# Performance work log

Hardware: AMD Instinct MI355X
Metric: run time of the kernel (lower is better)

Reference implementation:

```python
import jax, jax.numpy as jnp
import numpy as np

L = 4096      # number of nodes (treated as sequence length, batch=1)
D = 256       # in_channels == out_channels
H = 8         # heads
DH = D // H   # head dim = 32
NUM_EDGE_TYPES = 14


def setup_inputs() -> dict:
    key = jax.random.key(0)
    ks = jax.random.split(key, 7)
    x = jax.random.normal(ks[0], (L, D), dtype=jnp.float32)
    mask = jax.random.randint(ks[1], (L, L), 0, NUM_EDGE_TYPES, dtype=jnp.int64)
    s = 1.0 / np.sqrt(D)
    in_proj_w = jax.random.uniform(ks[2], (3 * D, D), jnp.float32, -s, s)
    in_proj_b = jnp.zeros((3 * D,), jnp.float32)
    out_proj_w = jax.random.uniform(ks[3], (D, D), jnp.float32, -s, s)
    out_proj_b = jnp.zeros((D,), jnp.float32)
    edge_bias = jax.random.normal(ks[4], (NUM_EDGE_TYPES, H), dtype=jnp.float32) * 0.02
    return {"x": x, "mask": mask, "in_proj_w": in_proj_w, "in_proj_b": in_proj_b,
            "out_proj_w": out_proj_w, "out_proj_b": out_proj_b, "edge_bias": edge_bias}


def reference(x, mask, in_proj_w, in_proj_b, out_proj_w, out_proj_b, edge_bias):
    # x: (L, D) node features -> viewed as batch-1 self-attention, edge-aware scores.
    qkv = x @ in_proj_w.T + in_proj_b                 # (L, 3D)
    q, k, v = jnp.split(qkv, 3, axis=-1)              # each (L, D)
    q = q.reshape(L, H, DH).transpose(1, 0, 2)        # (H, L, DH)
    k = k.reshape(L, H, DH).transpose(1, 0, 2)
    v = v.reshape(L, H, DH).transpose(1, 0, 2)
    scale = 1.0 / jnp.sqrt(jnp.asarray(DH, x.dtype))
    scores = jnp.einsum('hqd,hkd->hqk', q, k) * scale  # (H, L, L)
    # edge-type bias folded into attention scores: lookup (L,L)->(L,L,H)->(H,L,L)
    scores = scores + edge_bias[mask].transpose(2, 0, 1)
    attn = jax.nn.softmax(scores, axis=-1)             # (H, L, L)
    out = jnp.einsum('hqk,hkd->hqd', attn, v)          # (H, L, DH)
    out = out.transpose(1, 0, 2).reshape(L, D)         # merge heads
    return out @ out_proj_w.T + out_proj_b             # (L, D)
```

## Files before the change

### kernel.cpp

```cpp
#include <hip/hip_runtime.h>
#include <hip/hip_bf16.h>
#include <string.h>

#define L 4096
#define D 256
#define H 8
#define DH 32

typedef __attribute__((ext_vector_type(8))) short bf16x8;
typedef __attribute__((ext_vector_type(4))) float f32x4;

#define LOG2E 1.4426950408889634f
#define RS (0.17677669529663688f * LOG2E)

__device__ __forceinline__ ushort f2bf(float f) {
    union { float f; unsigned int i; } v; v.f = f;
    unsigned int x = v.i;
    return (ushort)((x + 0x7fffu + ((x >> 16) & 1u)) >> 16);
}
__device__ __forceinline__ bf16x8 cvt8(const float* p) {
    float4 a = *(const float4*)p;
    float4 b = *(const float4*)(p + 4);
    bf16x8 r;
    r[0] = (short)f2bf(a.x); r[1] = (short)f2bf(a.y);
    r[2] = (short)f2bf(a.z); r[3] = (short)f2bf(a.w);
    r[4] = (short)f2bf(b.x); r[5] = (short)f2bf(b.y);
    r[6] = (short)f2bf(b.z); r[7] = (short)f2bf(b.w);
    return r;
}
__device__ __forceinline__ unsigned int pkbf(float a, float b) {
    float2 t; t.x = a; t.y = b;
    __hip_bfloat162 r = __float22bfloat162_rn(t);
    unsigned int u; memcpy(&u, &r, 4);
    return u;
}

__device__ __forceinline__ int ksig(int u) {
    return 32 * (u >> 5) + 16 * ((u >> 2) & 1) + 4 * ((u >> 3) & 3) + (u & 3);
}

__global__ __launch_bounds__(256) void pack_kernel(
        const int* __restrict__ mask, const float* __restrict__ x,
        const float* __restrict__ wi, const float* __restrict__ wo,
        unsigned int* __restrict__ m2, ushort* __restrict__ xb,
        ushort* __restrict__ wib, ushort* __restrict__ wob)
{
    const int b = blockIdx.x;
    const int tid = threadIdx.x;
    if (b < 512) {
        __shared__ unsigned int rb[8 * 1025];
        const int4* src = (const int4*)(mask + (size_t)b * 8 * 4096);
#pragma unroll
        for (int i = 0; i < 32; i++) {
            const int g = i * 256 + tid;
            int4 v = src[g];
            rb[(g >> 10) * 1025 + (g & 1023)] =
                ((unsigned int)(v.x & 15) << 4)  | ((unsigned int)(v.y & 15) << 12) |
                ((unsigned int)(v.z & 15) << 20) | ((unsigned int)(v.w & 15) << 28);
        }
        __syncthreads();
        const int t = b >> 1, half = b & 1;
#pragma unroll
        for (int i = 0; i < 32; i++) {
            const int dd = i * 256 + tid;
            const int nt = dd & 3, s = (dd >> 2) & 7, qd = (dd >> 5) & 3, kt = dd >> 7;
            const unsigned int w =
                rb[s * 1025 + kt * 16 + 8 * (nt >> 1) + 2 * qd + (nt & 1)];
            m2[(size_t)t * 16384 + kt * 256 + (qd * 16 + 8 * half + s) * 4 + nt] = w;
        }
    } else if (b < 1024) {
        const int t = (b - 512) * 256 + tid;
        ((bf16x8*)xb)[t] = cvt8(x + t * 8);
    } else if (b < 1120) {
        const int t = (b - 1024) * 256 + tid;
        ((bf16x8*)wib)[t] = cvt8(wi + t * 8);
    } else {
        const int t = (b - 1120) * 256 + tid;
        ((bf16x8*)wob)[t] = cvt8(wo + t * 8);
    }
}

__global__ __launch_bounds__(256) void qkv_kernel(
        const ushort* __restrict__ xb, const ushort* __restrict__ wb,
        const float* __restrict__ b,
        ushort* __restrict__ Qb, ushort* __restrict__ Kb, ushort* __restrict__ Vt)
{
    const int lane = threadIdx.x & 63, wv = threadIdx.x >> 6;
    const int quad = lane >> 4, l15 = lane & 15;
    const int m0 = blockIdx.x * 64 + wv * 16;
    const int n0 = blockIdx.y * 64;

    f32x4 acc[4] = {};
    for (int ks = 0; ks < 8; ks++) {
        const int kd = ks * 32 + quad * 8;
        bf16x8 af = *(const bf16x8*)(xb + (m0 + l15) * D + kd);
#pragma unroll
        for (int nt = 0; nt < 4; nt++) {
            bf16x8 bfr = *(const bf16x8*)(wb + (n0 + nt * 16 + l15) * D + kd);
            acc[nt] = __builtin_amdgcn_mfma_f32_16x16x32_bf16(af, bfr, acc[nt], 0, 0, 0);
        }
    }
#pragma unroll
    for (int nt = 0; nt < 4; nt++) {
        const int j = n0 + nt * 16 + l15;
        const float bias = b[j];
#pragma unroll
        for (int r = 0; r < 4; r++) {
            const int row = m0 + quad * 4 + r;
            const float val = acc[nt][r] + bias;
            if (j < 256) {
                Qb[((j >> 5) * L + row) * DH + (j & 31)] = f2bf(val * RS);
            } else if (j < 512) {
                const int jj = j - 256;
                const int srow = (row & ~63) + ksig(row & 63);
                Kb[((jj >> 5) * L + srow) * DH + (jj & 31)] = f2bf(val);
            } else {
                const int jj = j - 512;
                Vt[((jj >> 5) * DH + (jj & 31)) * L + row] = f2bf(val);
            }
        }
    }
}

__global__ __launch_bounds__(512) void attn_kernel(
        const ushort* __restrict__ Qb, const ushort* __restrict__ Kb,
        const ushort* __restrict__ Vt, const unsigned char* __restrict__ m2,
        const float* __restrict__ edge_bias, ushort* __restrict__ Ob)
{
    __shared__ float ebt[16 * 64];
    __shared__ float red[7 * 1152];

    const int tid = threadIdx.x;
    const int lane = tid & 63, wv = tid >> 6;
    const int quad = lane >> 4, l15 = lane & 15;

    const int bid = blockIdx.x;
    const int xr = bid & 7, j = bid >> 3;
    const int qg = xr * 16 + (j >> 3);
    const int h  = j & 7;
    const int q0 = qg * 32;
    const int kt0 = wv * 8;

    {
        float* t = ebt + lane;
#pragma unroll
        for (int e = 0; e < 16; e++)
            t[e * 64] = (e < 14) ? edge_bias[e * H + h] * LOG2E : 0.f;
    }
    asm volatile("s_waitcnt lgkmcnt(0)" ::: "memory");

    const bf16x8 qfA = *(const bf16x8*)(Qb + (h * L + q0 + l15) * DH + quad * 8);
    const bf16x8 qfB = *(const bf16x8*)(Qb + (h * L + q0 + 16 + l15) * DH + quad * 8);
    const char* ebl = (const char*)(ebt + lane);

    const ushort* Kl = Kb + h * L * DH + kt0 * 64 * DH + l15 * DH + quad * 8;
    const ushort* Va = Vt + (h * DH + l15) * L + kt0 * 64 + quad * 8;
    const ushort* Vb = Vt + (h * DH + 16 + l15) * L + kt0 * 64 + quad * 8;
    const unsigned char* mpA = m2 + (size_t)(2 * qg) * 65536
                             + (size_t)kt0 * 1024 + lane * 16;
    const unsigned char* mpB = mpA + 65536;

    f32x4 o0A = {}, o1A = {}, osA = {};
    f32x4 o0B = {}, o1B = {}, osB = {};
    bf16x8 ones;
#pragma unroll
    for (int i = 0; i < 8; i++) ones[i] = (short)0x3F80;

    for (int kt = 0; kt < 8; kt++) {
        const int4 mA4 = *(const int4*)(mpA + kt * 1024);
        const int4 mB4 = *(const int4*)(mpB + kt * 1024);
        const unsigned int mA[4] = {(unsigned int)mA4.x, (unsigned int)mA4.y,
                                    (unsigned int)mA4.z, (unsigned int)mA4.w};
        const unsigned int mB[4] = {(unsigned int)mB4.x, (unsigned int)mB4.y,
                                    (unsigned int)mB4.z, (unsigned int)mB4.w};

#pragma unroll
        for (int half = 0; half < 2; half++) {
            union { bf16x8 v; unsigned int u[4]; } pfA, pfB;
#pragma unroll
            for (int nt2 = 0; nt2 < 2; nt2++) {
                const int nt = half * 2 + nt2;
                bf16x8 kf = *(const bf16x8*)(Kl + (kt * 64 + nt * 16) * DH);
                f32x4 z = {};
                f32x4 svA = __builtin_amdgcn_mfma_f32_16x16x32_bf16(kf, qfA, z, 0, 0, 0);
                f32x4 svB = __builtin_amdgcn_mfma_f32_16x16x32_bf16(kf, qfB, z, 0, 0, 0);
                const unsigned int wA = mA[nt], wB = mB[nt];
                float a0 = __builtin_amdgcn_exp2f(svA[0] + *(const float*)(ebl + ((wA        & 255u) << 4)));
                float a1 = __builtin_amdgcn_exp2f(svA[1] + *(const float*)(ebl + (((wA >> 8)  & 255u) << 4)));
                float a2 = __builtin_amdgcn_exp2f(svA[2] + *(const float*)(ebl + (((wA >> 16) & 255u) << 4)));
                float a3 = __builtin_amdgcn_exp2f(svA[3] + *(const float*)(ebl + ((wA >> 24)         << 4)));
                float b0 = __builtin_amdgcn_exp2f(svB[0] + *(const float*)(ebl + ((wB        & 255u) << 4)));
                float b1 = __builtin_amdgcn_exp2f(svB[1] + *(const float*)(ebl + (((wB >> 8)  & 255u) << 4)));
                float b2 = __builtin_amdgcn_exp2f(svB[2] + *(const float*)(ebl + (((wB >> 16) & 255u) << 4)));
                float b3 = __builtin_amdgcn_exp2f(svB[3] + *(const float*)(ebl + ((wB >> 24)         << 4)));
                pfA.u[nt2 * 2]     = pkbf(a0, a1);
                pfA.u[nt2 * 2 + 1] = pkbf(a2, a3);
                pfB.u[nt2 * 2]     = pkbf(b0, b1);
                pfB.u[nt2 * 2 + 1] = pkbf(b2, b3);
            }
            bf16x8 va = *(const bf16x8*)(Va + kt * 64 + half * 32);
            bf16x8 vb = *(const bf16x8*)(Vb + kt * 64 + half * 32);
            o0A = __builtin_amdgcn_mfma_f32_16x16x32_bf16(va,   pfA.v, o0A, 0, 0, 0);
            o1A = __builtin_amdgcn_mfma_f32_16x16x32_bf16(vb,   pfA.v, o1A, 0, 0, 0);
            osA = __builtin_amdgcn_mfma_f32_16x16x32_bf16(ones, pfA.v, osA, 0, 0, 0);
            o0B = __builtin_amdgcn_mfma_f32_16x16x32_bf16(va,   pfB.v, o0B, 0, 0, 0);
            o1B = __builtin_amdgcn_mfma_f32_16x16x32_bf16(vb,   pfB.v, o1B, 0, 0, 0);
            osB = __builtin_amdgcn_mfma_f32_16x16x32_bf16(ones, pfB.v, osB, 0, 0, 0);
        }
    }

    if (wv > 0) {
        float* s = red + (wv - 1) * 1152;
        *(f32x4*)(s +        lane * 4) = o0A;
        *(f32x4*)(s + 256  + lane * 4) = o1A;
        *(f32x4*)(s + 512  + lane * 4) = o0B;
        *(f32x4*)(s + 768  + lane * 4) = o1B;
        s[1024 + lane] = osA[0];
        s[1088 + lane] = osB[0];
    }
    __syncthreads();
    if (wv == 0) {
#pragma unroll
        for (int sl = 0; sl < 7; sl++) {
            const float* s = red + sl * 1152;
            o0A += *(const f32x4*)(s +        lane * 4);
            o1A += *(const f32x4*)(s + 256  + lane * 4);
            o0B += *(const f32x4*)(s + 512  + lane * 4);
            o1B += *(const f32x4*)(s + 768  + lane * 4);
            osA[0] += s[1024 + lane];
            osB[0] += s[1088 + lane];
        }
        const float invA = 1.f / osA[0];
        const float invB = 1.f / osB[0];
        ushort* orA = Ob + (size_t)(q0 + l15) * D + h * 32;
        ushort* orB = orA + (size_t)16 * D;
        uint2 u;
        u.x = pkbf(o0A[0] * invA, o0A[1] * invA);
        u.y = pkbf(o0A[2] * invA, o0A[3] * invA);
        *(uint2*)(orA + quad * 4) = u;
        u.x = pkbf(o1A[0] * invA, o1A[1] * invA);
        u.y = pkbf(o1A[2] * invA, o1A[3] * invA);
        *(uint2*)(orA + 16 + quad * 4) = u;
        u.x = pkbf(o0B[0] * invB, o0B[1] * invB);
        u.y = pkbf(o0B[2] * invB, o0B[3] * invB);
        *(uint2*)(orB + quad * 4) = u;
        u.x = pkbf(o1B[0] * invB, o1B[1] * invB);
        u.y = pkbf(o1B[2] * invB, o1B[3] * invB);
        *(uint2*)(orB + 16 + quad * 4) = u;
    }
}

__global__ __launch_bounds__(256) void oproj_kernel(
        const ushort* __restrict__ Ob, const ushort* __restrict__ wb,
        const float* __restrict__ b, float* __restrict__ out)
{
    const int lane = threadIdx.x & 63, wv = threadIdx.x >> 6;
    const int quad = lane >> 4, l15 = lane & 15;
    const int m0 = blockIdx.x * 64 + wv * 16;
    const int n0 = blockIdx.y * 64;

    f32x4 acc[4] = {};
    for (int ks = 0; ks < 8; ks++) {
        const int kd = ks * 32 + quad * 8;
        bf16x8 af = *(const bf16x8*)(Ob + (m0 + l15) * D + kd);
#pragma unroll
        for (int nt = 0; nt < 4; nt++) {
            bf16x8 bfr = *(const bf16x8*)(wb + (n0 + nt * 16 + l15) * D + kd);
            acc[nt] = __builtin_amdgcn_mfma_f32_16x16x32_bf16(af, bfr, acc[nt], 0, 0, 0);
        }
    }
#pragma unroll
    for (int nt = 0; nt < 4; nt++) {
        const int j = n0 + nt * 16 + l15;
        const float bias = b[j];
#pragma unroll
        for (int r = 0; r < 4; r++) {
            const int orow = m0 + quad * 4 + r;
            out[orow * D + j] = acc[nt][r] + bias;
        }
    }
}

extern "C" void kernel_launch(void* const* d_in, const int* in_sizes, int n_in,
                              void* d_out, int out_size, void* d_ws, size_t ws_size,
                              hipStream_t stream) {
    const float* x     = (const float*)d_in[0];
    const int*   mask  = (const int*)d_in[1];
    const float* in_w  = (const float*)d_in[2];
    const float* in_b  = (const float*)d_in[3];
    const float* out_w = (const float*)d_in[4];
    const float* out_b = (const float*)d_in[5];
    const float* eb    = (const float*)d_in[6];

    ushort* ws = (ushort*)d_ws;
    ushort* Qb  = ws;
    ushort* Kb  = Qb + H * L * DH;
    ushort* Vt  = Kb + H * L * DH;
    ushort* xb  = Vt + H * L * DH;
    ushort* wib = xb + L * D;
    ushort* wob = wib + 3 * D * D;
    unsigned char* m2 = (unsigned char*)(wob + D * D);
    ushort* Ob = (ushort*)(m2 + (size_t)L * L);
    float* out = (float*)d_out;

    pack_kernel<<<dim3(1152), 256, 0, stream>>>(mask, x, in_w, out_w,
                                                (unsigned int*)m2, xb, wib, wob);
    qkv_kernel<<<dim3(64, 12), 256, 0, stream>>>(xb, wib, in_b, Qb, Kb, Vt);
    attn_kernel<<<dim3(1024), 512, 0, stream>>>(Qb, Kb, Vt, m2, eb, Ob);
    oproj_kernel<<<dim3(64, 4), 256, 0, stream>>>(Ob, wob, out_b, out);
}
```

Baseline: 187.4 us.

## Pair edge types into a packed bf16 LUT and raise MFMA priority

```diff
diff --git a/kernel.cpp b/kernel.cpp
--- a/kernel.cpp
+++ b/kernel.cpp
@@ -33,6 +33,9 @@
     __hip_bfloat162 r = __float22bfloat162_rn(t);
     unsigned int u; memcpy(&u, &r, 4);
     return u;
+}
+__device__ __forceinline__ float uaf(unsigned int u) {
+    union { unsigned int u; float f; } v; v.u = u; return v.f;
 }
 
 __device__ __forceinline__ int ksig(int u) {
@@ -66,7 +69,11 @@
             const int nt = dd & 3, s = (dd >> 2) & 7, qd = (dd >> 5) & 3, kt = dd >> 7;
             const unsigned int w =
                 rb[s * 1025 + kt * 16 + 8 * (nt >> 1) + 2 * qd + (nt & 1)];
-            m2[(size_t)t * 16384 + kt * 256 + (qd * 16 + 8 * half + s) * 4 + nt] = w;
+            const unsigned int e0 = (w >> 4) & 15u, e1 = (w >> 12) & 15u;
+            const unsigned int e2 = (w >> 20) & 15u, e3 = w >> 28;
+            const unsigned int p01 = e0 * 14u + e1, p23 = e2 * 14u + e3;
+            m2[(size_t)t * 16384 + kt * 256 + (qd * 16 + 8 * half + s) * 4 + nt] =
+                (p01 << 6) | (p23 << 22);
         }
     } else if (b < 1024) {
         const int t = (b - 512) * 256 + tid;
@@ -127,7 +134,7 @@
         const ushort* __restrict__ Vt, const unsigned char* __restrict__ m2,
         const float* __restrict__ edge_bias, ushort* __restrict__ Ob)
 {
-    __shared__ float ebt[16 * 64];
+    __shared__ unsigned int lutp[196 * 16];
     __shared__ float red[7 * 1152];
 
     const int tid = threadIdx.x;
@@ -141,17 +148,18 @@
     const int q0 = qg * 32;
     const int kt0 = wv * 8;
 
-    {
-        float* t = ebt + lane;
-#pragma unroll
-        for (int e = 0; e < 16; e++)
-            t[e * 64] = (e < 14) ? edge_bias[e * H + h] * LOG2E : 0.f;
-    }
-    asm volatile("s_waitcnt lgkmcnt(0)" ::: "memory");
+    for (int i = tid; i < 196 * 16; i += 512) {
+        const int p = i >> 4;
+        const int e1 = (p * 2341) >> 15;
+        const int e2 = p - 14 * e1;
+        lutp[i] = pkbf(edge_bias[e1 * H + h] * LOG2E,
+                       edge_bias[e2 * H + h] * LOG2E);
+    }
+    __syncthreads();
 
     const bf16x8 qfA = *(const bf16x8*)(Qb + (h * L + q0 + l15) * DH + quad * 8);
     const bf16x8 qfB = *(const bf16x8*)(Qb + (h * L + q0 + 16 + l15) * DH + quad * 8);
-    const char* ebl = (const char*)(ebt + lane);
+    const char* lutb = (const char*)lutp + l15 * 4;
 
     const ushort* Kl = Kb + h * L * DH + kt0 * 64 * DH + l15 * DH + quad * 8;
     const ushort* Va = Vt + (h * DH + l15) * L + kt0 * 64 + quad * 8;
@@ -185,14 +193,18 @@
                 f32x4 svA = __builtin_amdgcn_mfma_f32_16x16x32_bf16(kf, qfA, z, 0, 0, 0);
                 f32x4 svB = __builtin_amdgcn_mfma_f32_16x16x32_bf16(kf, qfB, z, 0, 0, 0);
                 const unsigned int wA = mA[nt], wB = mB[nt];
-                float a0 = __builtin_amdgcn_exp2f(svA[0] + *(const float*)(ebl + ((wA        & 255u) << 4)));
-                float a1 = __builtin_amdgcn_exp2f(svA[1] + *(const float*)(ebl + (((wA >> 8)  & 255u) << 4)));
-                float a2 = __builtin_amdgcn_exp2f(svA[2] + *(const float*)(ebl + (((wA >> 16) & 255u) << 4)));
-                float a3 = __builtin_amdgcn_exp2f(svA[3] + *(const float*)(ebl + ((wA >> 24)         << 4)));
-                float b0 = __builtin_amdgcn_exp2f(svB[0] + *(const float*)(ebl + ((wB        & 255u) << 4)));
-                float b1 = __builtin_amdgcn_exp2f(svB[1] + *(const float*)(ebl + (((wB >> 8)  & 255u) << 4)));
-                float b2 = __builtin_amdgcn_exp2f(svB[2] + *(const float*)(ebl + (((wB >> 16) & 255u) << 4)));
-                float b3 = __builtin_amdgcn_exp2f(svB[3] + *(const float*)(ebl + ((wB >> 24)         << 4)));
+                const unsigned int dA0 = *(const unsigned int*)(lutb + (wA & 0xFFFFu));
+                const unsigned int dA1 = *(const unsigned int*)(lutb + (wA >> 16));
+                const unsigned int dB0 = *(const unsigned int*)(lutb + (wB & 0xFFFFu));
+                const unsigned int dB1 = *(const unsigned int*)(lutb + (wB >> 16));
+                float a0 = __builtin_amdgcn_exp2f(svA[0] + uaf(dA0 << 16));
+                float a1 = __builtin_amdgcn_exp2f(svA[1] + uaf(dA0 & 0xFFFF0000u));
+                float a2 = __builtin_amdgcn_exp2f(svA[2] + uaf(dA1 << 16));
+                float a3 = __builtin_amdgcn_exp2f(svA[3] + uaf(dA1 & 0xFFFF0000u));
+                float b0 = __builtin_amdgcn_exp2f(svB[0] + uaf(dB0 << 16));
+                float b1 = __builtin_amdgcn_exp2f(svB[1] + uaf(dB0 & 0xFFFF0000u));
+                float b2 = __builtin_amdgcn_exp2f(svB[2] + uaf(dB1 << 16));
+                float b3 = __builtin_amdgcn_exp2f(svB[3] + uaf(dB1 & 0xFFFF0000u));
                 pfA.u[nt2 * 2]     = pkbf(a0, a1);
                 pfA.u[nt2 * 2 + 1] = pkbf(a2, a3);
                 pfB.u[nt2 * 2]     = pkbf(b0, b1);
@@ -200,12 +212,14 @@
             }
             bf16x8 va = *(const bf16x8*)(Va + kt * 64 + half * 32);
             bf16x8 vb = *(const bf16x8*)(Vb + kt * 64 + half * 32);
+            __builtin_amdgcn_s_setprio(1);
             o0A = __builtin_amdgcn_mfma_f32_16x16x32_bf16(va,   pfA.v, o0A, 0, 0, 0);
             o1A = __builtin_amdgcn_mfma_f32_16x16x32_bf16(vb,   pfA.v, o1A, 0, 0, 0);
             osA = __builtin_amdgcn_mfma_f32_16x16x32_bf16(ones, pfA.v, osA, 0, 0, 0);
             o0B = __builtin_amdgcn_mfma_f32_16x16x32_bf16(va,   pfB.v, o0B, 0, 0, 0);
             o1B = __builtin_amdgcn_mfma_f32_16x16x32_bf16(vb,   pfB.v, o1B, 0, 0, 0);
             osB = __builtin_amdgcn_mfma_f32_16x16x32_bf16(ones, pfB.v, osB, 0, 0, 0);
+            __builtin_amdgcn_s_setprio(0);
         }
     }
 
```

New measurement: 185.1 us. Within noise of the previous version (-1.2%).
